# Kernel optimization log

Hardware: AMD Instinct MI355X
Metric: run time of the kernel (lower is better)

Reference implementation:

```python
import jax, jax.numpy as jnp
import numpy as np

# Model dims (see init_kwargs / shape_source)
B = 2048      # batch
CIN = 256     # tabular input features (c_in)
NH = 512      # TabularEncoder hidden width
NENC_HID = 4  # nlayers=6 -> input layer + 4 hidden + output layer
NF = 112      # n_features = num_concepts (conv=False path)
K = 112       # num_concepts
NL = 50       # num_latent_concepts
MC = 100      # num_monte_carlo
NOUT = 200    # num_output


def setup_inputs() -> dict:
    key = jax.random.key(0)
    ks = jax.random.split(key, 8)
    x = jax.random.normal(ks[0], (B, CIN), dtype=jnp.float32)
    enc_Win = jax.random.normal(ks[1], (CIN, NH), dtype=jnp.float32) * (1.0 / np.sqrt(CIN))
    enc_bin = jnp.zeros((NH,), jnp.float32)
    enc_Wh = jax.random.normal(ks[2], (NENC_HID, NH, NH), dtype=jnp.float32) * (1.0 / np.sqrt(NH))
    enc_bh = jnp.zeros((NENC_HID, NH), jnp.float32)
    enc_Wout = jax.random.normal(ks[3], (NH, NF), dtype=jnp.float32) * (1.0 / np.sqrt(NH))
    enc_bout = jnp.zeros((NF,), jnp.float32)
    # Per-concept predictor i has first Linear of shape [NF+i, NL]; pad all to [NF+K, NL]
    # and statically slice rows [:NF+i] in the loop (unused padded rows never touched).
    pred_W1 = jax.random.normal(ks[4], (K, NF + K, NL), dtype=jnp.float32) * (1.0 / np.sqrt(NF))
    pred_b1 = jnp.zeros((K, NL), jnp.float32)
    pred_W2 = jax.random.normal(ks[5], (K, NL), dtype=jnp.float32) * (1.0 / np.sqrt(NL))
    pred_b2 = jnp.zeros((K,), jnp.float32)
    head_W = jax.random.normal(ks[6], (K, NOUT), dtype=jnp.float32) * (1.0 / np.sqrt(K))
    head_b = jnp.zeros((NOUT,), jnp.float32)
    return {
        "x": x,
        "enc_Win": enc_Win, "enc_bin": enc_bin,
        "enc_Wh": enc_Wh, "enc_bh": enc_bh,
        "enc_Wout": enc_Wout, "enc_bout": enc_bout,
        "pred_W1": pred_W1, "pred_b1": pred_b1,
        "pred_W2": pred_W2, "pred_b2": pred_b2,
        "head_W": head_W, "head_b": head_b,
        "epoch": 0,
    }


def reference(x, enc_Win, enc_bin, enc_Wh, enc_bh, enc_Wout, enc_bout,
              pred_W1, pred_b1, pred_W2, pred_b2, head_W, head_b, epoch):
    lrelu = jax.nn.leaky_relu  # negative_slope=0.01, matches nn.LeakyReLU default

    # ---- TabularEncoder (ni=CIN, nhidden=NH, nlayers=6, no=NF) ----
    h = lrelu(x @ enc_Win + enc_bin)
    for i in range(enc_Wh.shape[0]):
        h = lrelu(h @ enc_Wh[i] + enc_bh[i])
    inter = h @ enc_Wout + enc_bout                      # [B, NF]
    Bn = inter.shape[0]

    key = jax.random.key(42)
    c_hard = jnp.zeros((Bn, K, MC), inter.dtype)
    c_probs = []
    for i in range(K):
        W1 = pred_W1[i, :NF + i]                          # [NF+i, NL]
        base = inter @ W1[:NF] + pred_b1[i]               # [B, NL], shared across MC
        if i == 0:
            p1 = jax.nn.sigmoid(lrelu(base) @ pred_W2[i] + pred_b2[i])   # [B]
            p = jnp.broadcast_to(p1[:, None], (Bn, MC))   # expand(-1,-1,MC)
        else:
            # add contribution of the i previously sampled hard concepts, per MC sample
            hpre = base[:, None, :] + jnp.einsum('bim,ih->bmh', c_hard[:, :i], W1[NF:])  # [B,MC,NL]
            p = jax.nn.sigmoid(jnp.einsum('bmh,h->bm', lrelu(hpre), pred_W2[i]) + pred_b2[i])  # [B,MC]
        key, sk = jax.random.split(key)
        samp = jax.random.bernoulli(sk, p).astype(p.dtype)  # torch.bernoulli(concept)
        c_hard = c_hard.at[:, i, :].set(samp)
        c_probs.append(p)

    c_prob = jnp.stack(c_probs, axis=1)                   # [B, K, MC]

    # ---- Head: MC average of softmax probabilities (pred_dim > 1 branch) ----
    logits = jnp.einsum('bkm,ko->bmo', c_hard, head_W) + head_b   # [B, MC, NOUT]
    probs = jax.nn.softmax(logits, axis=-1).mean(axis=1)          # [B, NOUT]
    y_pred_logits = jnp.log(probs + 1e-6)
    return (c_prob, y_pred_logits, c_hard)
```

## Files before the change

kernel.cpp:

```cpp
#include <hip/hip_runtime.h>

typedef unsigned int u32;
typedef unsigned short u16;
typedef unsigned long long u64;

#define YOFF  22937600ull
#define CHOFF 23347200ull

#define OFF_HA    0ull
#define OFF_HB    4194304ull
#define OFF_INTER 8388608ull

__host__ __device__ inline u32 rotl32_(u32 x, int r) { return (x << r) | (x >> (32 - r)); }
__host__ __device__ inline void tf2x32(u32 k0, u32 k1, u32 c0, u32 c1, u32& o0, u32& o1) {
  u32 ks0 = k0, ks1 = k1, ks2 = k0 ^ k1 ^ 0x1BD11BDAu;
  u32 x0 = c0 + ks0, x1 = c1 + ks1;
  const int RA[4] = {13, 15, 26, 6}, RB[4] = {17, 29, 16, 24};
  for (int i = 0; i < 5; ++i) {
    const int* R = (i & 1) ? RB : RA;
    for (int j = 0; j < 4; ++j) { x0 += x1; x1 = rotl32_(x1, R[j]); x1 ^= x0; }
    switch (i) {
      case 0: x0 += ks1; x1 += ks2 + 1u; break;
      case 1: x0 += ks2; x1 += ks0 + 2u; break;
      case 2: x0 += ks0; x1 += ks1 + 3u; break;
      case 3: x0 += ks1; x1 += ks2 + 4u; break;
      case 4: x0 += ks2; x1 += ks0 + 5u; break;
    }
  }
  o0 = x0; o1 = x1;
}

struct SKeys { u32 v[224]; };

template <bool DO_LRELU>
__global__ __launch_bounds__(256) void gemm_bias(const float* __restrict__ A,
                                                 const float* __restrict__ Bm,
                                                 const float* __restrict__ bias,
                                                 float* __restrict__ C,
                                                 int M, int N, int K) {
  __shared__ float As[32][65];
  __shared__ float Bs[32][65];
  const int bm = blockIdx.y * 64, bn = blockIdx.x * 64;
  const int t = threadIdx.x;
  const int ty = t >> 4, tx = t & 15;
  float acc[4][4] = {};
  for (int k0 = 0; k0 < K; k0 += 32) {
#pragma unroll
    for (int l = 0; l < 2; ++l) {
      int e = l * 256 + t;
      int m = e >> 3, k4 = e & 7;
      float4 v = *(const float4*)(A + (size_t)(bm + m) * K + (k0 + k4 * 4));
      As[k4 * 4 + 0][m] = v.x; As[k4 * 4 + 1][m] = v.y;
      As[k4 * 4 + 2][m] = v.z; As[k4 * 4 + 3][m] = v.w;
    }
#pragma unroll
    for (int l = 0; l < 2; ++l) {
      int e = l * 256 + t;
      int k = e >> 4, n4 = e & 15;
      int gn = bn + n4 * 4;
      if (gn < N) {
        float4 v = *(const float4*)(Bm + (size_t)(k0 + k) * N + gn);
        Bs[k][n4 * 4 + 0] = v.x; Bs[k][n4 * 4 + 1] = v.y;
        Bs[k][n4 * 4 + 2] = v.z; Bs[k][n4 * 4 + 3] = v.w;
      } else {
        Bs[k][n4 * 4 + 0] = 0.f; Bs[k][n4 * 4 + 1] = 0.f;
        Bs[k][n4 * 4 + 2] = 0.f; Bs[k][n4 * 4 + 3] = 0.f;
      }
    }
    __syncthreads();
#pragma unroll
    for (int kk = 0; kk < 32; ++kk) {
      float a[4], b[4];
#pragma unroll
      for (int j = 0; j < 4; ++j) { a[j] = As[kk][ty * 4 + j]; b[j] = Bs[kk][tx * 4 + j]; }
#pragma unroll
      for (int i = 0; i < 4; ++i)
#pragma unroll
        for (int j = 0; j < 4; ++j) acc[i][j] = fmaf(a[i], b[j], acc[i][j]);
    }
    __syncthreads();
  }
#pragma unroll
  for (int i = 0; i < 4; ++i) {
#pragma unroll
    for (int j = 0; j < 4; ++j) {
      int m = bm + ty * 4 + i, n = bn + tx * 4 + j;
      if (n < N) {
        float s = acc[i][j] + bias[n];
        if (DO_LRELU) { if (s < 0.f) s = 0.01f * s; }
        C[(size_t)m * N + n] = s;
      }
    }
  }
}

__global__ __launch_bounds__(256) void base_kernel(const float* __restrict__ inter,
                                                   const float* __restrict__ W1,
                                                   const float* __restrict__ pb1,
                                                   float* __restrict__ out) {
  __shared__ float As[112][65];
  __shared__ float Ws[112][64];
  const int i = blockIdx.y;
  const int b0 = blockIdx.x * 64;
  const int t = threadIdx.x;
  const int ty = t >> 4, tx = t & 15;
#pragma unroll
  for (int l = 0; l < 7; ++l) {
    int e4 = l * 256 + t;
    int k4 = e4 % 28, bs = e4 / 28;
    float4 v = *(const float4*)(inter + (size_t)(b0 + bs) * 112 + k4 * 4);
    As[k4 * 4 + 0][bs] = v.x; As[k4 * 4 + 1][bs] = v.y;
    As[k4 * 4 + 2][bs] = v.z; As[k4 * 4 + 3][bs] = v.w;
  }
#pragma unroll
  for (int l = 0; l < 28; ++l) {
    int e = l * 256 + t;
    int r = e >> 6, c = e & 63;
    Ws[r][c] = (c < 50) ? W1[(size_t)i * 11200 + r * 50 + c] : 0.f;
  }
  __syncthreads();
  float acc[4][4] = {};
  for (int kk = 0; kk < 112; ++kk) {
    float a[4], b[4];
#pragma unroll
    for (int j = 0; j < 4; ++j) { a[j] = As[kk][ty * 4 + j]; b[j] = Ws[kk][tx * 4 + j]; }
#pragma unroll
    for (int ii = 0; ii < 4; ++ii)
#pragma unroll
      for (int j = 0; j < 4; ++j) acc[ii][j] = fmaf(a[ii], b[j], acc[ii][j]);
  }
#pragma unroll
  for (int ii = 0; ii < 4; ++ii) {
#pragma unroll
    for (int j = 0; j < 4; ++j) {
      int b = b0 + ty * 4 + ii, h = tx * 4 + j;
      if (h < 50) {
        out[CHOFF + (size_t)b * 11200 + (size_t)i * 100 + h] = acc[ii][j] + pb1[i * 50 + h];
      }
    }
  }
}

__global__ __launch_bounds__(512) void sample_kernel(const float* __restrict__ W1,
                                                     const float* __restrict__ W2,
                                                     const float* __restrict__ b2,
                                                     float* __restrict__ out, SKeys sks) {
  const int t = threadIdx.x;
  const int p = blockIdx.x * 500 + t;
  const bool active = (t < 500) && (p < 204800);
  const int b = p / 100;
  const int m = p - b * 100;
  const size_t rowbase = (size_t)b * 11200 + m;
  const float* __restrict__ baserow = out + CHOFF + (size_t)b * 11200;
  u64 lo = 0, hi = 0;

  if (active) {
    for (int i = 0; i < 112; ++i) {
      const float* __restrict__ Wi = W1 + (size_t)i * 11200 + 5600;
      float acc[50];
#pragma unroll
      for (int h = 0; h < 50; ++h) acc[h] = 0.f;
      for (int r = 0; r < i; ++r) {
        float c = (((r < 64) ? (lo >> r) : (hi >> (r - 64))) & 1ull) ? 1.f : 0.f;
        const float* __restrict__ wr = Wi + r * 50;
#pragma unroll
        for (int h = 0; h < 50; ++h) acc[h] = fmaf(c, wr[h], acc[h]);
      }
      const float* __restrict__ w2 = W2 + i * 50;
      const float* bs = baserow + (size_t)i * 100;
      float s = 0.f;
#pragma unroll
      for (int h = 0; h < 50; ++h) {
        float v = acc[h] + bs[h];
        if (v < 0.f) v = 0.01f * v;
        s = fmaf(v, w2[h], s);
      }
      float l = s + b2[i];
      float pr = 1.f / (1.f + expf(-l));
      u32 a0, a1;
      tf2x32(sks.v[2 * i], sks.v[2 * i + 1], 0u, (u32)p, a0, a1);
      u32 fb = ((a0 ^ a1) >> 9) | 0x3F800000u;
      float u; __builtin_memcpy(&u, &fb, 4); u -= 1.f;
      int smp = (u < pr) ? 1 : 0;
      out[rowbase + (size_t)i * 100] = pr;
      if (smp) { if (i < 64) lo |= 1ull << i; else hi |= 1ull << (i - 64); }
    }
    for (int i = 0; i < 112; ++i) {
      u64 bit = (i < 64) ? (lo >> i) : (hi >> (i - 64));
      out[CHOFF + rowbase + (size_t)i * 100] = (bit & 1ull) ? 1.0f : 0.0f;
    }
  }
}

__global__ __launch_bounds__(256) void head_kernel(const float* __restrict__ HW,
                                                   const float* __restrict__ hb,
                                                   float* __restrict__ out) {
  __shared__ unsigned char cS[100][116];
  __shared__ float lgS[50][201];
  const int b = blockIdx.x;
  const int t = threadIdx.x;
  for (int e = t; e < 11200; e += 256) {
    int k = e / 100, m = e - k * 100;
    cS[m][k] = (out[CHOFF + (size_t)b * 11200 + (size_t)k * 100 + m] != 0.f) ? 1 : 0;
  }
  __syncthreads();
  float pacc = 0.f;
  for (int mh = 0; mh < 2; ++mh) {
    for (int l = 0; l < 3; ++l) {
      int tile = l * 256 + t;
      if (tile < 625) {
        int o0 = (tile % 25) * 8;
        int m0 = (tile / 25) * 2;
        float acc[2][8] = {};
        for (int k = 0; k < 112; ++k) {
          float4 wa = *(const float4*)(HW + (size_t)k * 200 + o0);
          float4 wb = *(const float4*)(HW + (size_t)k * 200 + o0 + 4);
          float w[8] = {wa.x, wa.y, wa.z, wa.w, wb.x, wb.y, wb.z, wb.w};
          float c0 = (float)cS[mh * 50 + m0][k];
          float c1 = (float)cS[mh * 50 + m0 + 1][k];
#pragma unroll
          for (int jo = 0; jo < 8; ++jo) {
            acc[0][jo] = fmaf(c0, w[jo], acc[0][jo]);
            acc[1][jo] = fmaf(c1, w[jo], acc[1][jo]);
          }
        }
#pragma unroll
        for (int im = 0; im < 2; ++im)
#pragma unroll
          for (int jo = 0; jo < 8; ++jo) {
            int o = o0 + jo;
            lgS[m0 + im][o] = acc[im][jo] + hb[o];
          }
      }
    }
    __syncthreads();
    if (t < 50) {
      int m = t;
      float mx = -3.0e38f;
      for (int o = 0; o < 200; ++o) mx = fmaxf(mx, lgS[m][o]);
      float s = 0.f;
      for (int o = 0; o < 200; ++o) {
        float e = expf(lgS[m][o] - mx);
        lgS[m][o] = e; s += e;
      }
      float inv = 1.f / s;
      for (int o = 0; o < 200; ++o) lgS[m][o] = lgS[m][o] * inv;
    }
    __syncthreads();
    if (t < 200) { for (int m = 0; m < 50; ++m) pacc += lgS[m][t]; }
    __syncthreads();
  }
  if (t < 200) {
    out[YOFF + (size_t)b * 200 + t] = logf(pacc / 100.f + 1e-6f);
  }
}

extern "C" void kernel_launch(void* const* d_in, const int* in_sizes, int n_in,
                              void* d_out, int out_size, void* d_ws, size_t ws_size,
                              hipStream_t stream) {
  const float* x    = (const float*)d_in[0];
  const float* Win  = (const float*)d_in[1];
  const float* bin  = (const float*)d_in[2];
  const float* Wh   = (const float*)d_in[3];
  const float* bh   = (const float*)d_in[4];
  const float* Wout = (const float*)d_in[5];
  const float* bout = (const float*)d_in[6];
  const float* pW1  = (const float*)d_in[7];
  const float* pb1  = (const float*)d_in[8];
  const float* pW2  = (const float*)d_in[9];
  const float* pb2  = (const float*)d_in[10];
  const float* hW   = (const float*)d_in[11];
  const float* hb   = (const float*)d_in[12];
  float* out = (float*)d_out;
  char* ws = (char*)d_ws;

  float* hA     = (float*)(ws + OFF_HA);
  float* hB     = (float*)(ws + OFF_HB);
  float* interB = (float*)(ws + OFF_INTER);

  gemm_bias<true ><<<dim3(8, 32), 256, 0, stream>>>(x,  Win,             bin,          hA,     2048, 512, 256);
  gemm_bias<true ><<<dim3(8, 32), 256, 0, stream>>>(hA, Wh + 0 * 262144, bh + 0 * 512, hB,     2048, 512, 512);
  gemm_bias<true ><<<dim3(8, 32), 256, 0, stream>>>(hB, Wh + 1 * 262144, bh + 1 * 512, hA,     2048, 512, 512);
  gemm_bias<true ><<<dim3(8, 32), 256, 0, stream>>>(hA, Wh + 2 * 262144, bh + 2 * 512, hB,     2048, 512, 512);
  gemm_bias<true ><<<dim3(8, 32), 256, 0, stream>>>(hB, Wh + 3 * 262144, bh + 3 * 512, hA,     2048, 512, 512);
  gemm_bias<false><<<dim3(2, 32), 256, 0, stream>>>(hA, Wout,            bout,         interB, 2048, 112, 512);

  base_kernel<<<dim3(32, 112), 256, 0, stream>>>(interB, pW1, pb1, out);

  SKeys sks;
  {
    u32 k0 = 0u, k1 = 42u;
    for (int i = 0; i < 112; ++i) {
      u32 nk0, nk1, s0, s1;
      tf2x32(k0, k1, 0u, 0u, nk0, nk1);
      tf2x32(k0, k1, 0u, 1u, s0, s1);
      sks.v[2 * i] = s0; sks.v[2 * i + 1] = s1;
      k0 = nk0; k1 = nk1;
    }
  }
  sample_kernel<<<410, 512, 0, stream>>>(pW1, pW2, pb2, out, sks);

  head_kernel<<<2048, 256, 0, stream>>>(hW, hb, out);
}
```

Baseline: 3.714 ms.

## Stage sampler weights in shared memory, shrink blocks, split hard-concept expansion

The sequential sampling kernel now runs 128-thread blocks (1600 blocks instead of 410×512). Each step cooperatively copies that concept's W1 rows into LDS with float2 loads, so threads read weights from shared memory instead of each issuing global loads. The bitmask-to-float expansion of c_hard moves into a separate kernel that reads per-thread masks from workspace, which keeps the writes from racing with the base values the sampler still reads from that region. In exchange, every concept step adds two block barriers, and the extra kernel launch plus the mask round-trip add cost.

```diff
diff --git a/kernel.cpp b/kernel.cpp
--- a/kernel.cpp
+++ b/kernel.cpp
@@ -10,6 +10,7 @@
 #define OFF_HA    0ull
 #define OFF_HB    4194304ull
 #define OFF_INTER 8388608ull
+#define OFF_MASK  9306112ull
 
 __host__ __device__ inline u32 rotl32_(u32 x, int r) { return (x << r) | (x >> (32 - r)); }
 __host__ __device__ inline void tf2x32(u32 k0, u32 k1, u32 c0, u32 c1, u32& o0, u32& o1) {
@@ -141,54 +142,79 @@
   }
 }
 
-__global__ __launch_bounds__(512) void sample_kernel(const float* __restrict__ W1,
+__global__ __launch_bounds__(128) void sample_kernel(const float* __restrict__ W1,
                                                      const float* __restrict__ W2,
                                                      const float* __restrict__ b2,
-                                                     float* __restrict__ out, SKeys sks) {
+                                                     float* __restrict__ out,
+                                                     u64* __restrict__ masks, SKeys sks) {
+  __shared__ float Wl[5550];
   const int t = threadIdx.x;
-  const int p = blockIdx.x * 500 + t;
-  const bool active = (t < 500) && (p < 204800);
+  const int p = blockIdx.x * 128 + t;
   const int b = p / 100;
   const int m = p - b * 100;
   const size_t rowbase = (size_t)b * 11200 + m;
   const float* __restrict__ baserow = out + CHOFF + (size_t)b * 11200;
   u64 lo = 0, hi = 0;
 
-  if (active) {
-    for (int i = 0; i < 112; ++i) {
-      const float* __restrict__ Wi = W1 + (size_t)i * 11200 + 5600;
-      float acc[50];
-#pragma unroll
-      for (int h = 0; h < 50; ++h) acc[h] = 0.f;
-      for (int r = 0; r < i; ++r) {
-        float c = (((r < 64) ? (lo >> r) : (hi >> (r - 64))) & 1ull) ? 1.f : 0.f;
-        const float* __restrict__ wr = Wi + r * 50;
-#pragma unroll
-        for (int h = 0; h < 50; ++h) acc[h] = fmaf(c, wr[h], acc[h]);
-      }
-      const float* __restrict__ w2 = W2 + i * 50;
-      const float* bs = baserow + (size_t)i * 100;
-      float s = 0.f;
-#pragma unroll
-      for (int h = 0; h < 50; ++h) {
-        float v = acc[h] + bs[h];
-        if (v < 0.f) v = 0.01f * v;
-        s = fmaf(v, w2[h], s);
-      }
-      float l = s + b2[i];
-      float pr = 1.f / (1.f + expf(-l));
-      u32 a0, a1;
-      tf2x32(sks.v[2 * i], sks.v[2 * i + 1], 0u, (u32)p, a0, a1);
-      u32 fb = ((a0 ^ a1) >> 9) | 0x3F800000u;
-      float u; __builtin_memcpy(&u, &fb, 4); u -= 1.f;
-      int smp = (u < pr) ? 1 : 0;
-      out[rowbase + (size_t)i * 100] = pr;
-      if (smp) { if (i < 64) lo |= 1ull << i; else hi |= 1ull << (i - 64); }
-    }
-    for (int i = 0; i < 112; ++i) {
-      u64 bit = (i < 64) ? (lo >> i) : (hi >> (i - 64));
-      out[CHOFF + rowbase + (size_t)i * 100] = (bit & 1ull) ? 1.0f : 0.0f;
-    }
+  for (int i = 0; i < 112; ++i) {
+    __syncthreads();
+    {
+      const float2* __restrict__ src = (const float2*)(W1 + (size_t)i * 11200 + 5600);
+      float2* dst = (float2*)Wl;
+      const int n2 = i * 25;
+      for (int e = t; e < n2; e += 128) dst[e] = src[e];
+    }
+    __syncthreads();
+
+    float acc[50];
+#pragma unroll
+    for (int h = 0; h < 50; ++h) acc[h] = 0.f;
+    for (int r = 0; r < i; ++r) {
+      float c = (((r < 64) ? (lo >> r) : (hi >> (r - 64))) & 1ull) ? 1.f : 0.f;
+      const float2* __restrict__ wr = (const float2*)(Wl + r * 50);
+#pragma unroll
+      for (int h2 = 0; h2 < 25; ++h2) {
+        float2 w = wr[h2];
+        acc[2 * h2]     = fmaf(c, w.x, acc[2 * h2]);
+        acc[2 * h2 + 1] = fmaf(c, w.y, acc[2 * h2 + 1]);
+      }
+    }
+    const float* __restrict__ w2 = W2 + i * 50;
+    const float2* __restrict__ bp2 = (const float2*)(baserow + (size_t)i * 100);
+    float s = 0.f;
+#pragma unroll
+    for (int h2 = 0; h2 < 25; ++h2) {
+      float2 bv = bp2[h2];
+      float v0 = acc[2 * h2] + bv.x;
+      if (v0 < 0.f) v0 = 0.01f * v0;
+      s = fmaf(v0, w2[2 * h2], s);
+      float v1 = acc[2 * h2 + 1] + bv.y;
+      if (v1 < 0.f) v1 = 0.01f * v1;
+      s = fmaf(v1, w2[2 * h2 + 1], s);
+    }
+    float l = s + b2[i];
+    float pr = 1.f / (1.f + expf(-l));
+    u32 a0, a1;
+    tf2x32(sks.v[2 * i], sks.v[2 * i + 1], 0u, (u32)p, a0, a1);
+    u32 fb = ((a0 ^ a1) >> 9) | 0x3F800000u;
+    float u; __builtin_memcpy(&u, &fb, 4); u -= 1.f;
+    int smp = (u < pr) ? 1 : 0;
+    out[rowbase + (size_t)i * 100] = pr;
+    if (smp) { if (i < 64) lo |= 1ull << i; else hi |= 1ull << (i - 64); }
+  }
+  masks[2 * p] = lo; masks[2 * p + 1] = hi;
+}
+
+__global__ __launch_bounds__(256) void expand_kernel(const u64* __restrict__ masks,
+                                                     float* __restrict__ out) {
+  const int p = blockIdx.x * 256 + threadIdx.x;
+  const int b = p / 100;
+  const int m = p - b * 100;
+  u64 lo = masks[2 * p], hi = masks[2 * p + 1];
+  size_t base = CHOFF + (size_t)b * 11200 + m;
+  for (int i = 0; i < 112; ++i) {
+    u64 bit = (i < 64) ? (lo >> i) : (hi >> (i - 64));
+    out[base + (size_t)i * 100] = (bit & 1ull) ? 1.0f : 0.0f;
   }
 }
 
@@ -277,6 +303,7 @@
   float* hA     = (float*)(ws + OFF_HA);
   float* hB     = (float*)(ws + OFF_HB);
   float* interB = (float*)(ws + OFF_INTER);
+  u64*   masks  = (u64*)(ws + OFF_MASK);
 
   gemm_bias<true ><<<dim3(8, 32), 256, 0, stream>>>(x,  Win,             bin,          hA,     2048, 512, 256);
   gemm_bias<true ><<<dim3(8, 32), 256, 0, stream>>>(hA, Wh + 0 * 262144, bh + 0 * 512, hB,     2048, 512, 512);
@@ -298,7 +325,8 @@
       k0 = nk0; k1 = nk1;
     }
   }
-  sample_kernel<<<410, 512, 0, stream>>>(pW1, pW2, pb2, out, sks);
+  sample_kernel<<<1600, 128, 0, stream>>>(pW1, pW2, pb2, out, masks, sks);
+  expand_kernel<<<800, 256, 0, stream>>>(masks, out);
 
   head_kernel<<<2048, 256, 0, stream>>>(hW, hb, out);
 }
```

New measurement: 4.117 ms. +10.8%, slower.
